# Performance work log

Hardware: AMD Instinct MI355X
Metric: run time of the kernel (lower is better)

The kernel has to match this reference:

```python
import jax, jax.numpy as jnp
import numpy as np
from jax import lax

DIM = 64
HEADS = 4
B, Q, V = 8, 128, 128


def _modrelu(z, b):
    m = jnp.abs(z)
    return z * (jax.nn.relu(m + b) / (m + 1e-5))


def _eunn_unitary(h, th1, ph1, th2, ph2, om):
    # tunable-style EUNN, capacity 2: even-pair rotations, odd-pair rotations, diagonal phase
    d = h.shape[-1]
    # layer 1: pairs (0,1),(2,3),...
    hp = h.reshape(*h.shape[:-1], d // 2, 2)
    a, b = hp[..., 0], hp[..., 1]
    c1, s1, e1 = jnp.cos(th1), jnp.sin(th1), jnp.exp(1j * ph1)
    h = jnp.stack([e1 * (c1 * a - s1 * b), s1 * a + c1 * b], -1).reshape(h.shape)
    # layer 2: pairs (1,2),(3,4),...,(d-3,d-2); endpoints pass through
    mid = h[..., 1:d - 1].reshape(*h.shape[:-1], d // 2 - 1, 2)
    a, b = mid[..., 0], mid[..., 1]
    c2, s2, e2 = jnp.cos(th2), jnp.sin(th2), jnp.exp(1j * ph2)
    mid2 = jnp.stack([e2 * (c2 * a - s2 * b), s2 * a + c2 * b], -1).reshape(*h.shape[:-1], d - 2)
    h = jnp.concatenate([h[..., :1], mid2, h[..., d - 1:]], -1)
    return h * jnp.exp(1j * om)


def _forward(queries, values, U_re, U_im, bias, theta1, phi1, theta2, phi2, omega, W_dense, b_dense):
    Bq, Qq, d = queries.shape
    Vv = values.shape[1]
    # quadratic (query, value) expansion -> [B*Q, V, 2d]
    dq = jnp.broadcast_to(queries[:, :, None, :], (Bq, Qq, Vv, d))
    dv = jnp.broadcast_to(values[:, None, :, :], (Bq, Qq, Vv, d))
    x = jnp.concatenate([dq, dv], -1).reshape(Bq * Qq, Vv, 2 * d)
    U = (U_re + 1j * U_im)  # [H, 2d, d] complex input kernel per head
    Ux = jnp.einsum('nvi,hij->hvnj', x.astype(jnp.complex64), U)  # [H, V, N, d]

    def run_head(Ux_h, t1, p1, t2, p2, om, bh):
        def step(h, u):
            h2 = _modrelu(_eunn_unitary(h, t1, p1, t2, p2, om) + u, bh)
            return h2, None
        h0 = jnp.zeros(Ux_h.shape[1:], dtype=jnp.complex64)  # [N, d]
        hT, _ = lax.scan(step, h0, Ux_h)
        return hT  # final state, as Keras RNN with return_sequences=False

    outs = jax.vmap(run_head)(Ux, theta1, phi1, theta2, phi2, omega, bias)  # [H, N, d]
    acc = jnp.real(outs).transpose(1, 0, 2).reshape(Bq * Qq, HEADS * d)
    y = acc @ W_dense + b_dense
    return y.reshape(Bq, Qq, d)


def setup_inputs() -> dict:
    key = jax.random.key(0)
    ks = jax.random.split(key, 12)
    pi = np.pi
    return {
        'queries': jax.random.normal(ks[0], (B, Q, DIM), jnp.float32),
        'values': jax.random.normal(ks[1], (B, V, DIM), jnp.float32),
        'U_re': jax.random.normal(ks[2], (HEADS, 2 * DIM, DIM), jnp.float32) * (1.0 / np.sqrt(2 * DIM)),
        'U_im': jax.random.normal(ks[3], (HEADS, 2 * DIM, DIM), jnp.float32) * (1.0 / np.sqrt(2 * DIM)),
        'bias': jax.random.normal(ks[4], (HEADS, DIM), jnp.float32) * 0.01,
        'theta1': jax.random.uniform(ks[5], (HEADS, DIM // 2), jnp.float32, -pi, pi),
        'phi1': jax.random.uniform(ks[6], (HEADS, DIM // 2), jnp.float32, -pi, pi),
        'theta2': jax.random.uniform(ks[7], (HEADS, DIM // 2 - 1), jnp.float32, -pi, pi),
        'phi2': jax.random.uniform(ks[8], (HEADS, DIM // 2 - 1), jnp.float32, -pi, pi),
        'omega': jax.random.uniform(ks[9], (HEADS, DIM), jnp.float32, -pi, pi),
        'W_dense': jax.random.normal(ks[10], (HEADS * DIM, DIM), jnp.float32) * (1.0 / np.sqrt(HEADS * DIM)),
        'b_dense': jnp.zeros((DIM,), jnp.float32),
    }


def reference(queries, values, U_re, U_im, bias, theta1, phi1, theta2, phi2, omega, W_dense, b_dense):
    return _forward(queries, values, U_re, U_im, bias, theta1, phi1, theta2, phi2, omega, W_dense, b_dense)
```

## Files before the change

kernel.cpp:

```cpp
#include <hip/hip_runtime.h>
#include <math.h>

#define DIM 64
#define HEADS 4
#define BB 8
#define QQ 128
#define VV 128
#define NN (BB*QQ)

__device__ __forceinline__ float dpp_swap1(float x) {
    return __int_as_float(__builtin_amdgcn_update_dpp(
        0, __float_as_int(x), 0xB1, 0xF, 0xF, true));
}
__device__ __forceinline__ float dpp_wshr1(float x) {
    return __int_as_float(__builtin_amdgcn_update_dpp(
        0, __float_as_int(x), 0x138, 0xF, 0xF, true));
}
__device__ __forceinline__ float dpp_wshl1(float x) {
    return __int_as_float(__builtin_amdgcn_update_dpp(
        0, __float_as_int(x), 0x130, 0xF, 0xF, true));
}

__global__ __launch_bounds__(256) void k_av(const float* __restrict__ values,
                                            const float* __restrict__ U_re,
                                            const float* __restrict__ U_im,
                                            float2* __restrict__ Av) {
    int tid = blockIdx.x * blockDim.x + threadIdx.x;
    int w = tid >> 6;
    int j = tid & 63;
    int h = __builtin_amdgcn_readfirstlane(w >> 10);
    int rem = __builtin_amdgcn_readfirstlane(w & 1023);
    const float* vrow = values + rem * DIM;
    const float* ur = U_re + (h * 2 * DIM + DIM) * DIM + j;
    const float* ui = U_im + (h * 2 * DIM + DIM) * DIM + j;
    float ar = 0.f, ai = 0.f;
    #pragma unroll 16
    for (int i = 0; i < DIM; ++i) {
        float vi = vrow[i];
        ar = fmaf(vi, ur[i * DIM], ar);
        ai = fmaf(vi, ui[i * DIM], ai);
    }
    Av[(h * 1024 + rem) * DIM + j] = make_float2(ar, ai);
}

__global__ __launch_bounds__(256) void k_rnn_dense(
        const float* __restrict__ queries,
        const float* __restrict__ U_re,
        const float* __restrict__ U_im,
        const float* __restrict__ bias,
        const float* __restrict__ theta1,
        const float* __restrict__ phi1,
        const float* __restrict__ theta2,
        const float* __restrict__ phi2,
        const float* __restrict__ omega,
        const float2* __restrict__ Av,
        const float* __restrict__ W_dense,
        const float* __restrict__ b_dense,
        float* __restrict__ y) {
    int b = blockIdx.x >> 6;
    int q = blockIdx.x & 63;
    int t = threadIdx.x;
    int h = t >> 6;
    int j = t & 63;
    int n0 = b * 128 + q;
    int n1 = n0 + 64;

    int k1 = j >> 1;
    float th1 = theta1[h * 32 + k1], ph1 = phi1[h * 32 + k1];
    float c1 = cosf(th1), s1 = sinf(th1);
    float A1r, A1i, B1r, B1i;
    if ((j & 1) == 0) {
        float er = cosf(ph1), ei = sinf(ph1);
        A1r = er * c1; A1i = ei * c1;
        B1r = -er * s1; B1i = -ei * s1;
    } else {
        A1r = c1; A1i = 0.f;
        B1r = s1; B1i = 0.f;
    }

    float A2r, A2i, BLr, BLi, BRr, BRi;
    if (j == 0 || j == 63) {
        A2r = 1.f; A2i = 0.f; BLr = 0.f; BLi = 0.f; BRr = 0.f; BRi = 0.f;
    } else {
        int k2 = (j - 1) >> 1;
        float th2 = theta2[h * 31 + k2], ph2 = phi2[h * 31 + k2];
        float c2 = cosf(th2), s2 = sinf(th2);
        if (j & 1) {
            float er = cosf(ph2), ei = sinf(ph2);
            A2r = er * c2; A2i = ei * c2;
            BLr = -er * s2; BLi = -ei * s2;
            BRr = 0.f; BRi = 0.f;
        } else {
            A2r = c2; A2i = 0.f;
            BRr = s2; BRi = 0.f;
            BLr = 0.f; BLi = 0.f;
        }
    }
    {
        float om = omega[h * 64 + j];
        float eor = cosf(om), eoi = sinf(om);
        float tr, ti;
        tr = A2r * eor - A2i * eoi; ti = A2r * eoi + A2i * eor; A2r = tr; A2i = ti;
        tr = BLr * eor - BLi * eoi; ti = BLr * eoi + BLi * eor; BLr = tr; BLi = ti;
        tr = BRr * eor - BRi * eoi; ti = BRr * eoi + BRi * eor; BRr = tr; BRi = ti;
    }
    float bj = bias[h * 64 + j];

    const float* qrow0 = queries + n0 * DIM;
    const float* qrow1 = queries + n1 * DIM;
    const float* ur = U_re + (h * 2 * DIM) * DIM + j;
    const float* ui = U_im + (h * 2 * DIM) * DIM + j;
    float uq0r = 0.f, uq0i = 0.f, uq1r = 0.f, uq1i = 0.f;
    #pragma unroll 16
    for (int i = 0; i < DIM; ++i) {
        float a0 = qrow0[i];
        float a1 = qrow1[i];
        float wr = ur[i * DIM], wi = ui[i * DIM];
        uq0r = fmaf(a0, wr, uq0r); uq0i = fmaf(a0, wi, uq0i);
        uq1r = fmaf(a1, wr, uq1r); uq1i = fmaf(a1, wi, uq1i);
    }

    const float2* Avp = Av + (h * 1024 + b * 128) * DIM + j;

    float h0r = 0.f, h0i = 0.f, h1r = 0.f, h1i = 0.f;
    #pragma unroll 4
    for (int v = 0; v < VV; ++v) {
        float2 av = Avp[v * DIM];
        {
            float pr = dpp_swap1(h0r), pi = dpp_swap1(h0i);
            float t_r = A1r * h0r - A1i * h0i + B1r * pr - B1i * pi;
            float t_i = A1r * h0i + A1i * h0r + B1r * pi + B1i * pr;
            float Lr = dpp_wshl1(t_r), Li = dpp_wshl1(t_i);
            float Rr = dpp_wshr1(t_r), Ri = dpp_wshr1(t_i);
            float s_r = A2r * t_r - A2i * t_i + BLr * Lr - BLi * Li + BRr * Rr - BRi * Ri;
            float s_i = A2r * t_i + A2i * t_r + BLr * Li + BLi * Lr + BRr * Ri + BRi * Rr;
            float zr = s_r + uq0r + av.x;
            float zi = s_i + uq0i + av.y;
            float q2 = fmaf(zr, zr, fmaf(zi, zi, 1e-30f));
            float rs = __builtin_amdgcn_rsqf(q2);
            float m = q2 * rs;
            float sc = fmaxf(m + bj, 0.f) * __builtin_amdgcn_rcpf(m + 1e-5f);
            h0r = zr * sc; h0i = zi * sc;
        }
        {
            float pr = dpp_swap1(h1r), pi = dpp_swap1(h1i);
            float t_r = A1r * h1r - A1i * h1i + B1r * pr - B1i * pi;
            float t_i = A1r * h1i + A1i * h1r + B1r * pi + B1i * pr;
            float Lr = dpp_wshl1(t_r), Li = dpp_wshl1(t_i);
            float Rr = dpp_wshr1(t_r), Ri = dpp_wshr1(t_i);
            float s_r = A2r * t_r - A2i * t_i + BLr * Lr - BLi * Li + BRr * Rr - BRi * Ri;
            float s_i = A2r * t_i + A2i * t_r + BLr * Li + BLi * Lr + BRr * Ri + BRi * Rr;
            float zr = s_r + uq1r + av.x;
            float zi = s_i + uq1i + av.y;
            float q2 = fmaf(zr, zr, fmaf(zi, zi, 1e-30f));
            float rs = __builtin_amdgcn_rsqf(q2);
            float m = q2 * rs;
            float sc = fmaxf(m + bj, 0.f) * __builtin_amdgcn_rcpf(m + 1e-5f);
            h1r = zr * sc; h1i = zi * sc;
        }
    }

    __shared__ float s_acc[2][HEADS * DIM];
    __shared__ float s_part[256];
    s_acc[0][h * 64 + j] = h0r;
    s_acc[1][h * 64 + j] = h1r;
    __syncthreads();

    {
        int r = t >> 7, hf = (t >> 6) & 1, jj = t & 63;
        const float* Wp = W_dense + (hf * 128) * DIM + jj;
        const float* ap = &s_acc[r][hf * 128];
        float part = 0.f;
        #pragma unroll 8
        for (int k = 0; k < 128; ++k)
            part = fmaf(ap[k], Wp[k * DIM], part);
        s_part[t] = part;
    }
    __syncthreads();
    if (t < 128) {
        int r = t >> 6, jj = t & 63;
        y[(n0 + r * 64) * DIM + jj] =
            b_dense[jj] + s_part[r * 128 + jj] + s_part[r * 128 + 64 + jj];
    }
}

extern "C" void kernel_launch(void* const* d_in, const int* in_sizes, int n_in,
                              void* d_out, int out_size, void* d_ws, size_t ws_size,
                              hipStream_t stream) {
    const float* queries = (const float*)d_in[0];
    const float* values  = (const float*)d_in[1];
    const float* U_re    = (const float*)d_in[2];
    const float* U_im    = (const float*)d_in[3];
    const float* bias    = (const float*)d_in[4];
    const float* theta1  = (const float*)d_in[5];
    const float* phi1    = (const float*)d_in[6];
    const float* theta2  = (const float*)d_in[7];
    const float* phi2    = (const float*)d_in[8];
    const float* omega   = (const float*)d_in[9];
    const float* W_dense = (const float*)d_in[10];
    const float* b_dense = (const float*)d_in[11];
    float* y = (float*)d_out;

    float2* Av = (float2*)d_ws;

    k_av<<<1024, 256, 0, stream>>>(values, U_re, U_im, Av);
    k_rnn_dense<<<512, 256, 0, stream>>>(queries, U_re, U_im, bias, theta1,
                                         phi1, theta2, phi2, omega, Av,
                                         W_dense, b_dense, y);
}
```

Baseline: 133.6 us.

## Pack RNN chains into float2 vectors for packed FP32 math and prefetch Av

Each thread's two recurrence chains are packed into 2-wide float vectors so the compiler can issue packed FP32 ops (v_pk_fma/v_pk_mul) on CDNA. The Av load for the next step is software-prefetched one iteration ahead. k_av now computes four value rows per thread with 4x fewer blocks, reusing each U load across rows. The aim is to halve the VALU instruction count in the latency-bound serial loop. The cost is extra register pressure, and possible repacking moves if the compiler does not keep the data in packed form.

```diff
diff --git a/kernel.cpp b/kernel.cpp
--- a/kernel.cpp
+++ b/kernel.cpp
@@ -8,6 +8,8 @@
 #define VV 128
 #define NN (BB*QQ)
 
+typedef float f2 __attribute__((ext_vector_type(2)));
+
 __device__ __forceinline__ float dpp_swap1(float x) {
     return __int_as_float(__builtin_amdgcn_update_dpp(
         0, __float_as_int(x), 0xB1, 0xF, 0xF, true));
@@ -20,27 +22,39 @@
     return __int_as_float(__builtin_amdgcn_update_dpp(
         0, __float_as_int(x), 0x130, 0xF, 0xF, true));
 }
+__device__ __forceinline__ f2 dpp2_swap1(f2 x) {
+    f2 r; r.x = dpp_swap1(x.x); r.y = dpp_swap1(x.y); return r;
+}
+__device__ __forceinline__ f2 dpp2_shl1(f2 x) {
+    f2 r; r.x = dpp_wshl1(x.x); r.y = dpp_wshl1(x.y); return r;
+}
+__device__ __forceinline__ f2 dpp2_shr1(f2 x) {
+    f2 r; r.x = dpp_wshr1(x.x); r.y = dpp_wshr1(x.y); return r;
+}
 
 __global__ __launch_bounds__(256) void k_av(const float* __restrict__ values,
                                             const float* __restrict__ U_re,
                                             const float* __restrict__ U_im,
-                                            float2* __restrict__ Av) {
+                                            f2* __restrict__ Av) {
     int tid = blockIdx.x * blockDim.x + threadIdx.x;
     int w = tid >> 6;
     int j = tid & 63;
-    int h = __builtin_amdgcn_readfirstlane(w >> 10);
-    int rem = __builtin_amdgcn_readfirstlane(w & 1023);
-    const float* vrow = values + rem * DIM;
+    int h = w >> 8;
+    int r0 = (w & 255) << 2;
+    const float* vrow = values + r0 * DIM;
     const float* ur = U_re + (h * 2 * DIM + DIM) * DIM + j;
     const float* ui = U_im + (h * 2 * DIM + DIM) * DIM + j;
-    float ar = 0.f, ai = 0.f;
-    #pragma unroll 16
+    f2 a0 = 0.f, a1 = 0.f, a2 = 0.f, a3 = 0.f;
+    #pragma unroll 8
     for (int i = 0; i < DIM; ++i) {
-        float vi = vrow[i];
-        ar = fmaf(vi, ur[i * DIM], ar);
-        ai = fmaf(vi, ui[i * DIM], ai);
-    }
-    Av[(h * 1024 + rem) * DIM + j] = make_float2(ar, ai);
+        f2 u; u.x = ur[i * DIM]; u.y = ui[i * DIM];
+        a0 += vrow[i] * u;
+        a1 += vrow[DIM + i] * u;
+        a2 += vrow[2 * DIM + i] * u;
+        a3 += vrow[3 * DIM + i] * u;
+    }
+    f2* out = Av + (h * 1024 + r0) * DIM + j;
+    out[0] = a0; out[DIM] = a1; out[2 * DIM] = a2; out[3 * DIM] = a3;
 }
 
 __global__ __launch_bounds__(256) void k_rnn_dense(
@@ -53,7 +67,7 @@
         const float* __restrict__ theta2,
         const float* __restrict__ phi2,
         const float* __restrict__ omega,
-        const float2* __restrict__ Av,
+        const f2* __restrict__ Av,
         const float* __restrict__ W_dense,
         const float* __restrict__ b_dense,
         float* __restrict__ y) {
@@ -110,60 +124,47 @@
     const float* qrow1 = queries + n1 * DIM;
     const float* ur = U_re + (h * 2 * DIM) * DIM + j;
     const float* ui = U_im + (h * 2 * DIM) * DIM + j;
-    float uq0r = 0.f, uq0i = 0.f, uq1r = 0.f, uq1i = 0.f;
-    #pragma unroll 16
+    f2 Uqr = 0.f, Uqi = 0.f;
+    #pragma unroll 8
     for (int i = 0; i < DIM; ++i) {
-        float a0 = qrow0[i];
-        float a1 = qrow1[i];
+        f2 a; a.x = qrow0[i]; a.y = qrow1[i];
         float wr = ur[i * DIM], wi = ui[i * DIM];
-        uq0r = fmaf(a0, wr, uq0r); uq0i = fmaf(a0, wi, uq0i);
-        uq1r = fmaf(a1, wr, uq1r); uq1i = fmaf(a1, wi, uq1i);
-    }
-
-    const float2* Avp = Av + (h * 1024 + b * 128) * DIM + j;
-
-    float h0r = 0.f, h0i = 0.f, h1r = 0.f, h1i = 0.f;
+        Uqr += a * wr;
+        Uqi += a * wi;
+    }
+
+    const f2* Avp = Av + (h * 1024 + b * 128) * DIM + j;
+
+    f2 Hr = 0.f, Hi = 0.f;
+    f2 av = Avp[0];
     #pragma unroll 4
     for (int v = 0; v < VV; ++v) {
-        float2 av = Avp[v * DIM];
-        {
-            float pr = dpp_swap1(h0r), pi = dpp_swap1(h0i);
-            float t_r = A1r * h0r - A1i * h0i + B1r * pr - B1i * pi;
-            float t_i = A1r * h0i + A1i * h0r + B1r * pi + B1i * pr;
-            float Lr = dpp_wshl1(t_r), Li = dpp_wshl1(t_i);
-            float Rr = dpp_wshr1(t_r), Ri = dpp_wshr1(t_i);
-            float s_r = A2r * t_r - A2i * t_i + BLr * Lr - BLi * Li + BRr * Rr - BRi * Ri;
-            float s_i = A2r * t_i + A2i * t_r + BLr * Li + BLi * Lr + BRr * Ri + BRi * Rr;
-            float zr = s_r + uq0r + av.x;
-            float zi = s_i + uq0i + av.y;
-            float q2 = fmaf(zr, zr, fmaf(zi, zi, 1e-30f));
-            float rs = __builtin_amdgcn_rsqf(q2);
-            float m = q2 * rs;
-            float sc = fmaxf(m + bj, 0.f) * __builtin_amdgcn_rcpf(m + 1e-5f);
-            h0r = zr * sc; h0i = zi * sc;
-        }
-        {
-            float pr = dpp_swap1(h1r), pi = dpp_swap1(h1i);
-            float t_r = A1r * h1r - A1i * h1i + B1r * pr - B1i * pi;
-            float t_i = A1r * h1i + A1i * h1r + B1r * pi + B1i * pr;
-            float Lr = dpp_wshl1(t_r), Li = dpp_wshl1(t_i);
-            float Rr = dpp_wshr1(t_r), Ri = dpp_wshr1(t_i);
-            float s_r = A2r * t_r - A2i * t_i + BLr * Lr - BLi * Li + BRr * Rr - BRi * Ri;
-            float s_i = A2r * t_i + A2i * t_r + BLr * Li + BLi * Lr + BRr * Ri + BRi * Rr;
-            float zr = s_r + uq1r + av.x;
-            float zi = s_i + uq1i + av.y;
-            float q2 = fmaf(zr, zr, fmaf(zi, zi, 1e-30f));
-            float rs = __builtin_amdgcn_rsqf(q2);
-            float m = q2 * rs;
-            float sc = fmaxf(m + bj, 0.f) * __builtin_amdgcn_rcpf(m + 1e-5f);
-            h1r = zr * sc; h1i = zi * sc;
-        }
+        f2 avn = Avp[((v + 1) & 127) * DIM];
+        f2 Pr = dpp2_swap1(Hr), Pi = dpp2_swap1(Hi);
+        f2 Tr = A1r * Hr - A1i * Hi + B1r * Pr - B1i * Pi;
+        f2 Ti = A1r * Hi + A1i * Hr + B1r * Pi + B1i * Pr;
+        f2 Lr = dpp2_shl1(Tr), Li = dpp2_shl1(Ti);
+        f2 Rr = dpp2_shr1(Tr), Ri = dpp2_shr1(Ti);
+        f2 Sr = A2r * Tr - A2i * Ti + BLr * Lr - BLi * Li + BRr * Rr - BRi * Ri;
+        f2 Si = A2r * Ti + A2i * Tr + BLr * Li + BLi * Lr + BRr * Ri + BRi * Rr;
+        f2 Zr = Sr + Uqr + av.x;
+        f2 Zi = Si + Uqi + av.y;
+        f2 q2 = Zr * Zr + Zi * Zi + 1e-30f;
+        f2 rs; rs.x = __builtin_amdgcn_rsqf(q2.x); rs.y = __builtin_amdgcn_rsqf(q2.y);
+        f2 m = q2 * rs;
+        f2 tp = m + bj;
+        tp.x = fmaxf(tp.x, 0.f); tp.y = fmaxf(tp.y, 0.f);
+        f2 mi = m + 1e-5f;
+        f2 inv; inv.x = __builtin_amdgcn_rcpf(mi.x); inv.y = __builtin_amdgcn_rcpf(mi.y);
+        f2 sc = tp * inv;
+        Hr = Zr * sc; Hi = Zi * sc;
+        av = avn;
     }
 
     __shared__ float s_acc[2][HEADS * DIM];
     __shared__ float s_part[256];
-    s_acc[0][h * 64 + j] = h0r;
-    s_acc[1][h * 64 + j] = h1r;
+    s_acc[0][h * 64 + j] = Hr.x;
+    s_acc[1][h * 64 + j] = Hr.y;
     __syncthreads();
 
     {
@@ -201,9 +202,9 @@
     const float* b_dense = (const float*)d_in[11];
     float* y = (float*)d_out;
 
-    float2* Av = (float2*)d_ws;
-
-    k_av<<<1024, 256, 0, stream>>>(values, U_re, U_im, Av);
+    f2* Av = (f2*)d_ws;
+
+    k_av<<<256, 256, 0, stream>>>(values, U_re, U_im, Av);
     k_rnn_dense<<<512, 256, 0, stream>>>(queries, U_re, U_im, bias, theta1,
                                          phi1, theta2, phi2, omega, Av,
                                          W_dense, b_dense, y);
```

New measurement: 120.0 us. 10.2% less time.
